# Performance work log

Measured on AMD Instinct MI355X. Metric: run time of the kernel, lower is better.

The kernel has to match this reference:

```python
import jax, jax.numpy as jnp
import numpy as np

DIM = 256
HEADS = 8
HEAD_DIM = DIM // HEADS
WH, WW = 8, 8
N = WH * WW
B = 4096
SCALE = HEAD_DIM ** -0.5


def _relative_position_index():
    ch = np.arange(WH)
    cw = np.arange(WW)
    coords = np.stack(np.meshgrid(ch, cw, indexing='ij'))  # [2, Wh, Ww]
    cf = coords.reshape(2, -1)                              # [2, N]
    rel = cf[:, :, None] - cf[:, None, :]                   # [2, N, N]
    rel = rel.transpose(1, 2, 0).copy()                     # [N, N, 2]
    rel[:, :, 0] += WH - 1
    rel[:, :, 1] += WW - 1
    rel[:, :, 0] *= 2 * WW - 1
    return jnp.asarray(rel.sum(-1), dtype=jnp.int32)        # [N, N]


def setup_inputs() -> dict:
    key = jax.random.key(0)
    ks = jax.random.split(key, 8)
    inner = HEADS * HEAD_DIM
    x = jax.random.normal(ks[0], (B, N, DIM), dtype=jnp.float32)
    wq = jax.random.normal(ks[1], (DIM, inner), dtype=jnp.float32) * 0.02
    bq = jnp.zeros((inner,), dtype=jnp.float32)
    wkv = jax.random.normal(ks[2], (DIM, 2 * inner), dtype=jnp.float32) * 0.02
    bkv = jnp.zeros((2 * inner,), dtype=jnp.float32)
    wp = jax.random.normal(ks[3], (DIM, DIM), dtype=jnp.float32) * 0.02
    bp = jnp.zeros((DIM,), dtype=jnp.float32)
    rpb_table = jax.random.normal(ks[4], ((2 * WH - 1) * (2 * WW - 1), HEADS), dtype=jnp.float32) * 0.02
    rel_idx = _relative_position_index()
    return {"x": x, "wq": wq, "bq": bq, "wkv": wkv, "bkv": bkv,
            "wp": wp, "bp": bp, "rpb_table": rpb_table, "rel_idx": rel_idx}


def reference(x, wq, bq, wkv, bkv, wp, bp, rpb_table, rel_idx):
    Bn, Nn, C = x.shape
    # q, k, v: [B, heads, N, head_dim]
    q = (x @ wq + bq).reshape(Bn, Nn, HEADS, HEAD_DIM).transpose(0, 2, 1, 3)
    kv = (x @ wkv + bkv).reshape(Bn, Nn, 2, HEADS, HEAD_DIM).transpose(2, 0, 3, 1, 4)
    k, v = kv[0], kv[1]
    q = q * SCALE
    attn = jnp.einsum('bhnd,bhmd->bhnm', q, k)  # [B, h, N, N]
    bias = rpb_table[rel_idx]                   # [N, N, h]
    bias = bias.transpose(2, 0, 1)              # [h, N, N] (ratio == 1 here)
    attn = jax.nn.softmax(attn + bias[None], axis=-1)
    out = jnp.einsum('bhnm,bhmd->bhnd', attn, v)
    out = out.transpose(0, 2, 1, 3).reshape(Bn, Nn, C)
    return out @ wp + bp
```

## Files before the change

### kernel.cpp

```cpp
#include <hip/hip_runtime.h>

typedef __attribute__((ext_vector_type(8))) _Float16 half8;
typedef __attribute__((ext_vector_type(4))) float f32x4;

#define MFMA16(a,b,c) __builtin_amdgcn_mfma_f32_16x16x32_f16(a, b, c, 0, 0, 0)

__global__ void prep_kernel(const float* __restrict__ wq, const float* __restrict__ bq,
                            const float* __restrict__ wkv, const float* __restrict__ bkv,
                            const float* __restrict__ wp, const float* __restrict__ rpb,
                            const int* __restrict__ rel,
                            _Float16* __restrict__ wqkvT, _Float16* __restrict__ wpT,
                            float* __restrict__ bqkv, float* __restrict__ biasg)
{
    int idx = blockIdx.x * 256 + threadIdx.x;
    const float scale = 0.17677669529663687f;
    if (idx < 196608) {
        int c = idx >> 8, k = idx & 255;
        int h = c / 96, r = c % 96;
        float v;
        if (r < 32)      v = wq[k*256 + h*32 + r] * scale;
        else if (r < 64) v = wkv[k*512 + h*32 + (r-32)];
        else             v = wkv[k*512 + 256 + h*32 + (r-64)];
        wqkvT[c*256 + k] = (_Float16)v;
    } else if (idx < 262144) {
        int i = idx - 196608;
        int n = i >> 8, k = i & 255;
        wpT[i] = (_Float16)wp[k*256 + n];
    } else if (idx < 262912) {
        int c = idx - 262144;
        int h = c / 96, r = c % 96;
        float v;
        if (r < 32)      v = bq[h*32 + r] * scale;
        else if (r < 64) v = bkv[h*32 + (r-32)];
        else             v = bkv[256 + h*32 + (r-64)];
        bqkv[c] = v;
    } else if (idx < 295680) {
        int i = idx - 262912;
        int h = i >> 12, rc = i & 4095;
        biasg[i] = rpb[rel[rc]*8 + h];
    }
}

__global__ __launch_bounds__(256, 2)
void attn_main(const float* __restrict__ x,
               const _Float16* __restrict__ wqkvT,
               const _Float16* __restrict__ wpT,
               const float* __restrict__ bqkv,
               const float* __restrict__ biasg,
               const float* __restrict__ bp,
               float* __restrict__ out)
{
    __shared__ _Float16 sx[64*264];
    __shared__ _Float16 sq[2][64*40];
    __shared__ _Float16 sk[2][64*40];
    __shared__ _Float16 sv[2][32*72];
    __shared__ _Float16 sP[64*72];
    __shared__ _Float16 sO[64*72];

    const int tid  = threadIdx.x;
    const int w    = tid >> 6;
    const int lane = tid & 63;
    const int l15  = lane & 15;
    const int quad = lane >> 4;
    const int b    = blockIdx.x;

    const float* xb = x + (size_t)b * (64*256);

    #pragma unroll
    for (int i = 0; i < 16; ++i) {
        int c4  = i*256 + tid;
        int row = c4 >> 6;
        int col = (c4 & 63) << 2;
        float4 v = ((const float4*)xb)[c4];
        union { _Float16 h[4]; uint2 u2; } pk;
        pk.h[0] = (_Float16)v.x; pk.h[1] = (_Float16)v.y;
        pk.h[2] = (_Float16)v.z; pk.h[3] = (_Float16)v.w;
        *(uint2*)(&sx[row*264 + col]) = pk.u2;
    }

    f32x4 dacc[4][4];
    #pragma unroll
    for (int i = 0; i < 4; ++i)
        #pragma unroll
        for (int j = 0; j < 4; ++j)
            dacc[i][j] = (f32x4){0.f, 0.f, 0.f, 0.f};

    __syncthreads();

    for (int pair = 0; pair < 4; ++pair) {
        f32x4 acc[3][4];
        #pragma unroll
        for (int nt = 0; nt < 3; ++nt)
            #pragma unroll
            for (int mt = 0; mt < 4; ++mt)
                acc[nt][mt] = (f32x4){0.f, 0.f, 0.f, 0.f};

        #pragma unroll
        for (int ks = 0; ks < 8; ++ks) {
            half8 af[4];
            #pragma unroll
            for (int mt = 0; mt < 4; ++mt)
                af[mt] = *(const half8*)&sx[(16*mt + l15)*264 + ks*32 + quad*8];
            #pragma unroll
            for (int nt = 0; nt < 3; ++nt) {
                int gcol = pair*192 + w*48 + nt*16 + l15;
                half8 bf = *(const half8*)(wqkvT + (size_t)gcol*256 + ks*32 + quad*8);
                #pragma unroll
                for (int mt = 0; mt < 4; ++mt)
                    acc[nt][mt] = MFMA16(af[mt], bf, acc[nt][mt]);
            }
        }
        #pragma unroll
        for (int nt = 0; nt < 3; ++nt) {
            int seg = w*48 + nt*16;
            float bv = bqkv[pair*192 + seg + l15];
            int hs  = (seg >= 96) ? 1 : 0;
            int r   = seg - 96*hs;
            int ty  = r >> 5;
            int ds_ = r & 31;
            #pragma unroll
            for (int mt = 0; mt < 4; ++mt) {
                #pragma unroll
                for (int rg = 0; rg < 4; ++rg) {
                    _Float16 hv = (_Float16)(acc[nt][mt][rg] + bv);
                    int token = 16*mt + quad*4 + rg;
                    if (ty == 0)      sq[hs][token*40 + ds_ + l15] = hv;
                    else if (ty == 1) sk[hs][token*40 + ds_ + l15] = hv;
                    else              sv[hs][(ds_ + l15)*72 + token] = hv;
                }
            }
        }
        __syncthreads();

        for (int hh = 0; hh < 2; ++hh) {
            int h = pair*2 + hh;
            float bb[4][4];
            #pragma unroll
            for (int rg = 0; rg < 4; ++rg) {
                const float* bg = biasg + ((h*64) + 16*w + quad*4 + rg)*64 + l15;
                bb[rg][0] = bg[0];  bb[rg][1] = bg[16];
                bb[rg][2] = bg[32]; bb[rg][3] = bg[48];
            }
            half8 aq = *(const half8*)&sq[hh][(16*w + l15)*40 + quad*8];
            f32x4 s[4];
            #pragma unroll
            for (int nt = 0; nt < 4; ++nt) {
                half8 bk = *(const half8*)&sk[hh][(16*nt + l15)*40 + quad*8];
                s[nt] = MFMA16(aq, bk, ((f32x4){0.f,0.f,0.f,0.f}));
            }
            float rinv[4];
            #pragma unroll
            for (int rg = 0; rg < 4; ++rg) {
                int row = quad*4 + rg;
                float t0 = s[0][rg] + bb[rg][0];
                float t1 = s[1][rg] + bb[rg][1];
                float t2 = s[2][rg] + bb[rg][2];
                float t3 = s[3][rg] + bb[rg][3];
                float m = fmaxf(fmaxf(t0, t1), fmaxf(t2, t3));
                #pragma unroll
                for (int d = 1; d < 16; d <<= 1)
                    m = fmaxf(m, __shfl_xor(m, d));
                float e0 = __expf(t0 - m), e1 = __expf(t1 - m);
                float e2 = __expf(t2 - m), e3 = __expf(t3 - m);
                float sum = e0 + e1 + e2 + e3;
                #pragma unroll
                for (int d = 1; d < 16; d <<= 1)
                    sum += __shfl_xor(sum, d);
                rinv[rg] = 1.0f / sum;
                int prow = (16*w + row)*72;
                sP[prow +  0 + l15] = (_Float16)e0;
                sP[prow + 16 + l15] = (_Float16)e1;
                sP[prow + 32 + l15] = (_Float16)e2;
                sP[prow + 48 + l15] = (_Float16)e3;
            }
            f32x4 o[2];
            o[0] = o[1] = (f32x4){0.f,0.f,0.f,0.f};
            #pragma unroll
            for (int ks = 0; ks < 2; ++ks) {
                half8 ap = *(const half8*)&sP[(16*w + l15)*72 + ks*32 + quad*8];
                #pragma unroll
                for (int nt = 0; nt < 2; ++nt) {
                    half8 bv_ = *(const half8*)&sv[hh][(16*nt + l15)*72 + ks*32 + quad*8];
                    o[nt] = MFMA16(ap, bv_, o[nt]);
                }
            }
            #pragma unroll
            for (int nt = 0; nt < 2; ++nt)
                #pragma unroll
                for (int rg = 0; rg < 4; ++rg)
                    sO[(16*w + quad*4 + rg)*72 + hh*32 + nt*16 + l15] =
                        (_Float16)(o[nt][rg] * rinv[rg]);
        }
        __syncthreads();

        half8 aO[4][2];
        #pragma unroll
        for (int mt = 0; mt < 4; ++mt)
            #pragma unroll
            for (int ks = 0; ks < 2; ++ks)
                aO[mt][ks] = *(const half8*)&sO[(16*mt + l15)*72 + ks*32 + quad*8];
        #pragma unroll
        for (int nt = 0; nt < 4; ++nt) {
            #pragma unroll
            for (int ks = 0; ks < 2; ++ks) {
                half8 bw = *(const half8*)(wpT + (size_t)(64*w + 16*nt + l15)*256
                                           + pair*64 + ks*32 + quad*8);
                #pragma unroll
                for (int mt = 0; mt < 4; ++mt)
                    dacc[mt][nt] = MFMA16(aO[mt][ks], bw, dacc[mt][nt]);
            }
        }
    }

    float* sxf = (float*)sx;
    float* ob  = out + (size_t)b * (64*256);
    float4 bpv = ((const float4*)bp)[lane];
    #pragma unroll
    for (int chunk = 0; chunk < 2; ++chunk) {
        if (chunk) __syncthreads();
        #pragma unroll
        for (int mt2 = 0; mt2 < 2; ++mt2) {
            int mt = chunk*2 + mt2;
            #pragma unroll
            for (int nt = 0; nt < 4; ++nt)
                #pragma unroll
                for (int rg = 0; rg < 4; ++rg)
                    sxf[(16*mt2 + quad*4 + rg)*264 + 64*w + 16*nt + l15] = dacc[mt][nt][rg];
        }
        __syncthreads();
        #pragma unroll
        for (int i = 0; i < 8; ++i) {
            int row = i*4 + w;
            float4 vv = *(const float4*)&sxf[row*264 + 4*lane];
            vv.x += bpv.x; vv.y += bpv.y; vv.z += bpv.z; vv.w += bpv.w;
            *(float4*)&ob[(size_t)(chunk*32 + row)*256 + 4*lane] = vv;
        }
    }
}

extern "C" void kernel_launch(void* const* d_in, const int* in_sizes, int n_in,
                              void* d_out, int out_size, void* d_ws, size_t ws_size,
                              hipStream_t stream)
{
    const float* x   = (const float*)d_in[0];
    const float* wq  = (const float*)d_in[1];
    const float* bq  = (const float*)d_in[2];
    const float* wkv = (const float*)d_in[3];
    const float* bkv = (const float*)d_in[4];
    const float* wp  = (const float*)d_in[5];
    const float* bp  = (const float*)d_in[6];
    const float* rpb = (const float*)d_in[7];
    const int*   rel = (const int*)d_in[8];

    char* ws = (char*)d_ws;
    _Float16* wqkvT = (_Float16*)(ws);
    _Float16* wpT   = (_Float16*)(ws + 393216);
    float*    bqkv  = (float*)(ws + 524288);
    float*    biasg = (float*)(ws + 527360);

    hipLaunchKernelGGL(prep_kernel, dim3(1155), dim3(256), 0, stream,
                       wq, bq, wkv, bkv, wp, rpb, rel, wqkvT, wpT, bqkv, biasg);
    hipLaunchKernelGGL(attn_main, dim3(4096), dim3(256), 0, stream,
                       x, wqkvT, wpT, bqkv, biasg, bp, (float*)d_out);
}
```

Measured before the change: 755.0 us.

## Swap MFMA operand order to get transposed accumulators and vectorized LDS stores

Computes the QKV projection, QK^T and PV MFMAs with swapped A/B operands so each lane holds four consecutive columns of a row. Q, K, V, P and O can then be written to LDS as packed 8-byte stores instead of scalar half stores, and the bias loads become float4. Each softmax row now sits in one lane group, so the max and sum reductions need two cross-lane shuffles instead of four per row. P is normalized before the PV product rather than scaling O afterwards. The cost is extra per-wave branching, since the odd waves handle K and V tiles with different operand orders.

```diff
diff --git a/kernel.cpp b/kernel.cpp
--- a/kernel.cpp
+++ b/kernel.cpp
@@ -85,6 +85,8 @@
         for (int j = 0; j < 4; ++j)
             dacc[i][j] = (f32x4){0.f, 0.f, 0.f, 0.f};
 
+    const bool wodd = (w & 1);
+
     __syncthreads();
 
     for (int pair = 0; pair < 4; ++pair) {
@@ -101,32 +103,80 @@
             #pragma unroll
             for (int mt = 0; mt < 4; ++mt)
                 af[mt] = *(const half8*)&sx[(16*mt + l15)*264 + ks*32 + quad*8];
+            half8 bf[3];
             #pragma unroll
             for (int nt = 0; nt < 3; ++nt) {
                 int gcol = pair*192 + w*48 + nt*16 + l15;
-                half8 bf = *(const half8*)(wqkvT + (size_t)gcol*256 + ks*32 + quad*8);
+                bf[nt] = *(const half8*)(wqkvT + (size_t)gcol*256 + ks*32 + quad*8);
+            }
+            if (!wodd) {
+                #pragma unroll
+                for (int nt = 0; nt < 3; ++nt)
+                    #pragma unroll
+                    for (int mt = 0; mt < 4; ++mt)
+                        acc[nt][mt] = MFMA16(bf[nt], af[mt], acc[nt][mt]);
+            } else {
                 #pragma unroll
                 for (int mt = 0; mt < 4; ++mt)
-                    acc[nt][mt] = MFMA16(af[mt], bf, acc[nt][mt]);
-            }
-        }
-        #pragma unroll
-        for (int nt = 0; nt < 3; ++nt) {
-            int seg = w*48 + nt*16;
-            float bv = bqkv[pair*192 + seg + l15];
-            int hs  = (seg >= 96) ? 1 : 0;
-            int r   = seg - 96*hs;
-            int ty  = r >> 5;
-            int ds_ = r & 31;
-            #pragma unroll
-            for (int mt = 0; mt < 4; ++mt) {
-                #pragma unroll
-                for (int rg = 0; rg < 4; ++rg) {
-                    _Float16 hv = (_Float16)(acc[nt][mt][rg] + bv);
-                    int token = 16*mt + quad*4 + rg;
-                    if (ty == 0)      sq[hs][token*40 + ds_ + l15] = hv;
-                    else if (ty == 1) sk[hs][token*40 + ds_ + l15] = hv;
-                    else              sv[hs][(ds_ + l15)*72 + token] = hv;
+                    acc[0][mt] = MFMA16(bf[0], af[mt], acc[0][mt]);
+                #pragma unroll
+                for (int nt = 1; nt < 3; ++nt)
+                    #pragma unroll
+                    for (int mt = 0; mt < 4; ++mt)
+                        acc[nt][mt] = MFMA16(af[mt], bf[nt], acc[nt][mt]);
+            }
+        }
+
+        if (!wodd) {
+            #pragma unroll
+            for (int nt = 0; nt < 3; ++nt) {
+                int seg = w*48 + nt*16;
+                int hs  = (seg >= 96) ? 1 : 0;
+                int r   = seg - 96*hs;
+                int ty  = r >> 5;
+                int ds_ = (r & 31) + 4*quad;
+                float4 bv4 = *(const float4*)(bqkv + pair*192 + seg + 4*quad);
+                _Float16* dst = (ty == 0) ? sq[hs] : sk[hs];
+                #pragma unroll
+                for (int mt = 0; mt < 4; ++mt) {
+                    union { _Float16 h[4]; uint2 u2; } pk;
+                    pk.h[0] = (_Float16)(acc[nt][mt][0] + bv4.x);
+                    pk.h[1] = (_Float16)(acc[nt][mt][1] + bv4.y);
+                    pk.h[2] = (_Float16)(acc[nt][mt][2] + bv4.z);
+                    pk.h[3] = (_Float16)(acc[nt][mt][3] + bv4.w);
+                    *(uint2*)&dst[(16*mt + l15)*40 + ds_] = pk.u2;
+                }
+            }
+        } else {
+            {
+                int seg = w*48;
+                int hs  = (seg >= 96) ? 1 : 0;
+                int ds_ = ((seg - 96*hs) & 31) + 4*quad;
+                float4 bv4 = *(const float4*)(bqkv + pair*192 + seg + 4*quad);
+                #pragma unroll
+                for (int mt = 0; mt < 4; ++mt) {
+                    union { _Float16 h[4]; uint2 u2; } pk;
+                    pk.h[0] = (_Float16)(acc[0][mt][0] + bv4.x);
+                    pk.h[1] = (_Float16)(acc[0][mt][1] + bv4.y);
+                    pk.h[2] = (_Float16)(acc[0][mt][2] + bv4.z);
+                    pk.h[3] = (_Float16)(acc[0][mt][3] + bv4.w);
+                    *(uint2*)&sk[hs][(16*mt + l15)*40 + ds_] = pk.u2;
+                }
+            }
+            #pragma unroll
+            for (int nt = 1; nt < 3; ++nt) {
+                int seg = w*48 + nt*16;
+                int hs  = (seg >= 96) ? 1 : 0;
+                int ds_ = (seg - 96*hs) & 31;
+                float bv = bqkv[pair*192 + seg + l15];
+                #pragma unroll
+                for (int mt = 0; mt < 4; ++mt) {
+                    union { _Float16 h[4]; uint2 u2; } pk;
+                    pk.h[0] = (_Float16)(acc[nt][mt][0] + bv);
+                    pk.h[1] = (_Float16)(acc[nt][mt][1] + bv);
+                    pk.h[2] = (_Float16)(acc[nt][mt][2] + bv);
+                    pk.h[3] = (_Float16)(acc[nt][mt][3] + bv);
+                    *(uint2*)&sv[hs][(ds_ + l15)*72 + 16*mt + 4*quad] = pk.u2;
                 }
             }
         }
@@ -134,62 +184,80 @@
 
         for (int hh = 0; hh < 2; ++hh) {
             int h = pair*2 + hh;
-            float bb[4][4];
-            #pragma unroll
-            for (int rg = 0; rg < 4; ++rg) {
-                const float* bg = biasg + ((h*64) + 16*w + quad*4 + rg)*64 + l15;
-                bb[rg][0] = bg[0];  bb[rg][1] = bg[16];
-                bb[rg][2] = bg[32]; bb[rg][3] = bg[48];
-            }
+            const float* bgq = biasg + ((h*64) + 16*w + l15)*64 + 4*quad;
+            float4 bb[4];
+            #pragma unroll
+            for (int nt = 0; nt < 4; ++nt)
+                bb[nt] = *(const float4*)(bgq + 16*nt);
+
             half8 aq = *(const half8*)&sq[hh][(16*w + l15)*40 + quad*8];
             f32x4 s[4];
             #pragma unroll
             for (int nt = 0; nt < 4; ++nt) {
                 half8 bk = *(const half8*)&sk[hh][(16*nt + l15)*40 + quad*8];
-                s[nt] = MFMA16(aq, bk, ((f32x4){0.f,0.f,0.f,0.f}));
-            }
-            float rinv[4];
-            #pragma unroll
-            for (int rg = 0; rg < 4; ++rg) {
-                int row = quad*4 + rg;
-                float t0 = s[0][rg] + bb[rg][0];
-                float t1 = s[1][rg] + bb[rg][1];
-                float t2 = s[2][rg] + bb[rg][2];
-                float t3 = s[3][rg] + bb[rg][3];
-                float m = fmaxf(fmaxf(t0, t1), fmaxf(t2, t3));
-                #pragma unroll
-                for (int d = 1; d < 16; d <<= 1)
-                    m = fmaxf(m, __shfl_xor(m, d));
-                float e0 = __expf(t0 - m), e1 = __expf(t1 - m);
-                float e2 = __expf(t2 - m), e3 = __expf(t3 - m);
-                float sum = e0 + e1 + e2 + e3;
-                #pragma unroll
-                for (int d = 1; d < 16; d <<= 1)
-                    sum += __shfl_xor(sum, d);
-                rinv[rg] = 1.0f / sum;
-                int prow = (16*w + row)*72;
-                sP[prow +  0 + l15] = (_Float16)e0;
-                sP[prow + 16 + l15] = (_Float16)e1;
-                sP[prow + 32 + l15] = (_Float16)e2;
-                sP[prow + 48 + l15] = (_Float16)e3;
-            }
+                s[nt] = MFMA16(bk, aq, ((f32x4){0.f,0.f,0.f,0.f}));
+            }
+
+            float t[4][4];
+            #pragma unroll
+            for (int nt = 0; nt < 4; ++nt) {
+                t[nt][0] = s[nt][0] + bb[nt].x;
+                t[nt][1] = s[nt][1] + bb[nt].y;
+                t[nt][2] = s[nt][2] + bb[nt].z;
+                t[nt][3] = s[nt][3] + bb[nt].w;
+            }
+            float mx = t[0][0];
+            #pragma unroll
+            for (int nt = 0; nt < 4; ++nt)
+                #pragma unroll
+                for (int rg = 0; rg < 4; ++rg)
+                    mx = fmaxf(mx, t[nt][rg]);
+            mx = fmaxf(mx, __shfl_xor(mx, 16));
+            mx = fmaxf(mx, __shfl_xor(mx, 32));
+            float e[4][4];
+            float sm = 0.f;
+            #pragma unroll
+            for (int nt = 0; nt < 4; ++nt)
+                #pragma unroll
+                for (int rg = 0; rg < 4; ++rg) {
+                    e[nt][rg] = __expf(t[nt][rg] - mx);
+                    sm += e[nt][rg];
+                }
+            sm += __shfl_xor(sm, 16);
+            sm += __shfl_xor(sm, 32);
+            float rinv = 1.0f / sm;
+
+            int prow = (16*w + l15)*72;
+            #pragma unroll
+            for (int nt = 0; nt < 4; ++nt) {
+                union { _Float16 h[4]; uint2 u2; } pk;
+                pk.h[0] = (_Float16)(e[nt][0] * rinv);
+                pk.h[1] = (_Float16)(e[nt][1] * rinv);
+                pk.h[2] = (_Float16)(e[nt][2] * rinv);
+                pk.h[3] = (_Float16)(e[nt][3] * rinv);
+                *(uint2*)&sP[prow + 16*nt + 4*quad] = pk.u2;
+            }
+
             f32x4 o[2];
             o[0] = o[1] = (f32x4){0.f,0.f,0.f,0.f};
             #pragma unroll
             for (int ks = 0; ks < 2; ++ks) {
-                half8 ap = *(const half8*)&sP[(16*w + l15)*72 + ks*32 + quad*8];
+                half8 ap = *(const half8*)&sP[prow + ks*32 + quad*8];
                 #pragma unroll
                 for (int nt = 0; nt < 2; ++nt) {
                     half8 bv_ = *(const half8*)&sv[hh][(16*nt + l15)*72 + ks*32 + quad*8];
-                    o[nt] = MFMA16(ap, bv_, o[nt]);
-                }
-            }
-            #pragma unroll
-            for (int nt = 0; nt < 2; ++nt)
-                #pragma unroll
-                for (int rg = 0; rg < 4; ++rg)
-                    sO[(16*w + quad*4 + rg)*72 + hh*32 + nt*16 + l15] =
-                        (_Float16)(o[nt][rg] * rinv[rg]);
+                    o[nt] = MFMA16(bv_, ap, o[nt]);
+                }
+            }
+            #pragma unroll
+            for (int nt = 0; nt < 2; ++nt) {
+                union { _Float16 h[4]; uint2 u2; } pk;
+                pk.h[0] = (_Float16)o[nt][0];
+                pk.h[1] = (_Float16)o[nt][1];
+                pk.h[2] = (_Float16)o[nt][2];
+                pk.h[3] = (_Float16)o[nt][3];
+                *(uint2*)&sO[(16*w + l15)*72 + hh*32 + 16*nt + 4*quad] = pk.u2;
+            }
         }
         __syncthreads();
 
```

Result: faster. 699.6 us (-7.3%).
